# Optimization experiments

Measured on AMD Instinct MI355X. Metric: run time of the kernel, lower is better.

The kernel has to match this reference:

```python
import jax, jax.numpy as jnp
import numpy as np

H = 2048      # hidden_size
C = 256       # controller_hidden
B = 8192      # batch (tokens)
DT = 0.1


def setup_inputs() -> dict:
    key = jax.random.key(0)
    ks = jax.random.split(key, 8)
    h = jax.random.normal(ks[0], (B, H), dtype=jnp.float32)
    v = jax.random.normal(ks[1], (B, H), dtype=jnp.float32)
    # controller_in: Linear(2H -> C)
    W_in = jax.random.normal(ks[2], (C, 2 * H), dtype=jnp.float32) / np.sqrt(2 * H)
    b_in = jax.random.normal(ks[3], (C,), dtype=jnp.float32) * 0.01
    # controller_out: Linear(C -> 3H), weight ~ N(0, 0.01); bias init [2.2, -2.2, 0.0] per split
    W_out = jax.random.normal(ks[4], (3 * H, C), dtype=jnp.float32) * 0.01
    b_out = jnp.concatenate([
        jnp.full((H,), 2.2, dtype=jnp.float32),
        jnp.full((H,), -2.2, dtype=jnp.float32),
        jnp.zeros((H,), dtype=jnp.float32),
    ])
    # mu_proj: Linear(H -> H, bias=False); init zeros in module, use small random for a non-trivial baseline
    W_mu = jax.random.normal(ks[5], (H, H), dtype=jnp.float32) * 0.01
    mu = jnp.zeros((H,), dtype=jnp.float32)
    return {"h": h, "v": v, "W_in": W_in, "b_in": b_in, "W_out": W_out,
            "b_out": b_out, "W_mu": W_mu, "mu": mu}


def reference(h, v, W_in, b_in, W_out, b_out, W_mu, mu):
    hv = jnp.concatenate([h, v], axis=-1)                    # [B, 2H]
    ctrl = jax.nn.silu(hv @ W_in.T + b_in)                   # [B, C]
    ctrl_out = ctrl @ W_out.T + b_out                        # [B, 3H]
    alpha_raw, beta_raw, gate_raw = jnp.split(ctrl_out, 3, axis=-1)
    alpha = jax.nn.sigmoid(alpha_raw)
    beta = jnp.minimum(jax.nn.softplus(beta_raw), 2.0)
    gate = jax.nn.sigmoid(gate_raw)
    mu_contextual = mu + h @ W_mu.T                          # [B, H]
    error = h - mu_contextual
    v_next = jnp.clip(alpha * v - beta * error, -10.0, 10.0)
    h_next = h + DT * gate * v_next
    return h_next, v_next, mu_contextual
```

## Files before the change

### kernel.cpp

```cpp
#include <hip/hip_runtime.h>
#include <cstdint>
#include <cstddef>

#define B_TOK 8192
#define HDIM  2048
#define CDIM  256
#define KHV   4096
#define N3H   6144
#define DT_C  0.1f

typedef __bf16 bf16x8 __attribute__((ext_vector_type(8)));
typedef float  f32x4  __attribute__((ext_vector_type(4)));

typedef __attribute__((address_space(1))) void as1_void;
typedef __attribute__((address_space(3))) void as3_void;

__device__ __forceinline__ void g2l16(const void* g, void* l) {
    __builtin_amdgcn_global_load_lds((as1_void*)(void*)(uintptr_t)(g),
                                     (as3_void*)l, 16, 0, 0);
}

__device__ __forceinline__ unsigned short f2bf(float f) {
    unsigned int u = __float_as_uint(f);
    u += 0x7fffu + ((u >> 16) & 1u);
    return (unsigned short)(u >> 16);
}

__device__ __forceinline__ float bf2f(unsigned short s) {
    return __uint_as_float((unsigned int)s << 16);
}

__device__ __forceinline__ float fsigmoid(float x) {
    return __builtin_amdgcn_rcpf(1.f + __expf(-x));
}
__device__ __forceinline__ float fsoftplus(float x) {
    float t = __expf(-fabsf(x));
    return fmaxf(x, 0.f) + 0.69314718056f * __log2f(1.f + t);
}

__global__ void k_convert(const float* __restrict__ hp, const float* __restrict__ vp,
                          const float* __restrict__ Win, const float* __restrict__ Wout,
                          const float* __restrict__ Wmu,
                          ushort4* __restrict__ hv_b, ushort4* __restrict__ Wmu_b,
                          ushort4* __restrict__ Wout_b, ushort4* __restrict__ Win_b)
{
    const int HV_V   = B_TOK * KHV / 4;
    const int WMU_V  = HDIM * HDIM / 4;
    const int WOUT_V = N3H * CDIM / 4;
    const int WIN_V  = CDIM * KHV / 4;
    const int TOT    = HV_V + WMU_V + WOUT_V + WIN_V;
    for (int i = blockIdx.x * blockDim.x + threadIdx.x; i < TOT;
         i += gridDim.x * blockDim.x) {
        float4 x;
        ushort4* dst;
        if (i < HV_V) {
            int b  = i >> 10;
            int c4 = i & 1023;
            x = (c4 < 512) ? ((const float4*)hp)[b * 512 + c4]
                           : ((const float4*)vp)[b * 512 + (c4 - 512)];
            dst = hv_b + i;
        } else if (i < HV_V + WMU_V) {
            int j = i - HV_V;
            x = ((const float4*)Wmu)[j];
            dst = Wmu_b + j;
        } else if (i < HV_V + WMU_V + WOUT_V) {
            int j = i - (HV_V + WMU_V);
            x = ((const float4*)Wout)[j];
            dst = Wout_b + j;
        } else {
            int j = i - (HV_V + WMU_V + WOUT_V);
            x = ((const float4*)Win)[j];
            dst = Win_b + j;
        }
        ushort4 o;
        o.x = f2bf(x.x); o.y = f2bf(x.y); o.z = f2bf(x.z); o.w = f2bf(x.w);
        *dst = o;
    }
}

__global__ __launch_bounds__(256, 2)
void k_mid(const unsigned short* __restrict__ hvb,
           const unsigned short* __restrict__ Winb,
           const unsigned short* __restrict__ Wmub,
           const float* __restrict__ b_in,
           const float* __restrict__ mu,
           unsigned short* __restrict__ ctrl,
           float* __restrict__ outmu)
{
    __shared__ unsigned short sA[128 * 32];
    __shared__ unsigned short sB[128 * 32];
    const int tid  = threadIdx.x;
    const int wid  = tid >> 6;
    const int lane = tid & 63;
    const int quad = lane >> 4;
    const int l15  = lane & 15;
    const int wm   = wid >> 1, wn = wid & 1;
    const int srow = lane >> 2;
    const int sk   = (lane & 3) * 8;

    if (blockIdx.x < 512) {
        const int s  = (blockIdx.x & 7) * 64 + (blockIdx.x >> 3);
        const int bm = (s >> 2) * 64;
        const int bn = (s & 3) * 64;

        f32x4 acc[2][2];
#pragma unroll
        for (int a = 0; a < 2; ++a)
#pragma unroll
            for (int b = 0; b < 2; ++b) acc[a][b] = (f32x4){0.f, 0.f, 0.f, 0.f};

        const unsigned short* Ag = hvb  + (size_t)(bm + wid * 16 + srow) * KHV + sk;
        const unsigned short* Bg = Winb + (size_t)(bn + wid * 16 + srow) * KHV + sk;
        unsigned short* lA = &sA[(wid * 16) * 32];
        unsigned short* lB = &sB[(wid * 16) * 32];

        for (int kt = 0; kt < KHV; kt += 32) {
            g2l16(Ag + kt, lA);
            g2l16(Bg + kt, lB);
            __syncthreads();
            bf16x8 aF[2], bF[2];
#pragma unroll
            for (int t = 0; t < 2; ++t)
                aF[t] = *(const bf16x8*)&sA[(wm * 32 + t * 16 + l15) * 32 + quad * 8];
#pragma unroll
            for (int t = 0; t < 2; ++t)
                bF[t] = *(const bf16x8*)&sB[(wn * 32 + t * 16 + l15) * 32 + quad * 8];
#pragma unroll
            for (int tm = 0; tm < 2; ++tm)
#pragma unroll
                for (int tn = 0; tn < 2; ++tn)
                    acc[tm][tn] = __builtin_amdgcn_mfma_f32_16x16x32_bf16(
                        aF[tm], bF[tn], acc[tm][tn], 0, 0, 0);
            __syncthreads();
        }

#pragma unroll
        for (int tm = 0; tm < 2; ++tm)
#pragma unroll
            for (int tn = 0; tn < 2; ++tn) {
                const int n = bn + wn * 32 + tn * 16 + l15;
                const float bias = b_in[n];
#pragma unroll
                for (int r = 0; r < 4; ++r) {
                    const int m = bm + wm * 32 + tm * 16 + quad * 4 + r;
                    float x = acc[tm][tn][r] + bias;
                    float s2 = x * fsigmoid(x);
                    ctrl[(size_t)m * CDIM + n] = f2bf(s2);
                }
            }
    } else {
        const int t3  = blockIdx.x - 512;
        const int t3s = (t3 & 7) * 128 + (t3 >> 3);
        const int bm  = (t3s & 63) * 128;
        const int bn  = (t3s >> 6) * 128;

        f32x4 acc[4][4];
#pragma unroll
        for (int a = 0; a < 4; ++a)
#pragma unroll
            for (int b = 0; b < 4; ++b) acc[a][b] = (f32x4){0.f, 0.f, 0.f, 0.f};

        const unsigned short* Ag0 = hvb  + (size_t)(bm + wid * 16 + srow) * KHV + sk;
        const unsigned short* Ag1 = hvb  + (size_t)(bm + (wid + 4) * 16 + srow) * KHV + sk;
        const unsigned short* Bg0 = Wmub + (size_t)(bn + wid * 16 + srow) * HDIM + sk;
        const unsigned short* Bg1 = Wmub + (size_t)(bn + (wid + 4) * 16 + srow) * HDIM + sk;
        unsigned short* lA0 = &sA[(wid * 16) * 32];
        unsigned short* lA1 = &sA[((wid + 4) * 16) * 32];
        unsigned short* lB0 = &sB[(wid * 16) * 32];
        unsigned short* lB1 = &sB[((wid + 4) * 16) * 32];

        for (int kt = 0; kt < HDIM; kt += 32) {
            g2l16(Ag0 + kt, lA0);
            g2l16(Ag1 + kt, lA1);
            g2l16(Bg0 + kt, lB0);
            g2l16(Bg1 + kt, lB1);
            __syncthreads();
            bf16x8 aF[4], bF[4];
#pragma unroll
            for (int t = 0; t < 4; ++t)
                aF[t] = *(const bf16x8*)&sA[(wm * 64 + t * 16 + l15) * 32 + quad * 8];
#pragma unroll
            for (int t = 0; t < 4; ++t)
                bF[t] = *(const bf16x8*)&sB[(wn * 64 + t * 16 + l15) * 32 + quad * 8];
#pragma unroll
            for (int tm = 0; tm < 4; ++tm)
#pragma unroll
                for (int tn = 0; tn < 4; ++tn)
                    acc[tm][tn] = __builtin_amdgcn_mfma_f32_16x16x32_bf16(
                        aF[tm], bF[tn], acc[tm][tn], 0, 0, 0);
            __syncthreads();
        }

#pragma unroll
        for (int tm = 0; tm < 4; ++tm)
#pragma unroll
            for (int tn = 0; tn < 4; ++tn) {
                const int n = bn + wn * 64 + tn * 16 + l15;
                const float mub = mu[n];
#pragma unroll
                for (int r = 0; r < 4; ++r) {
                    const int m = bm + wm * 64 + tm * 16 + quad * 4 + r;
                    outmu[(size_t)m * HDIM + n] = acc[tm][tn][r] + mub;
                }
            }
    }
}

__global__ __launch_bounds__(256, 4)
void k_gemm2(const unsigned short* __restrict__ A,
             const unsigned short* __restrict__ Bw,
             const float* __restrict__ b_out,
             const unsigned short* __restrict__ hv,
             const float* __restrict__ mu_ctx,
             float* __restrict__ outp)
{
    __shared__ unsigned short sA[64 * 32];
    __shared__ unsigned short sB[3][64 * 32];
    const int tid  = threadIdx.x;
    const int wid  = tid >> 6;
    const int lane = tid & 63;
    const int quad = lane >> 4;
    const int l15  = lane & 15;
    const int wm   = wid >> 1, wn = wid & 1;
    const int bm   = blockIdx.x * 64;
    const int bn   = blockIdx.y * 64;
    const int srow = lane >> 2;
    const int sk   = (lane & 3) * 8;

    f32x4 acc[3][2][2];
#pragma unroll
    for (int p = 0; p < 3; ++p)
#pragma unroll
        for (int a = 0; a < 2; ++a)
#pragma unroll
            for (int b = 0; b < 2; ++b) acc[p][a][b] = (f32x4){0.f, 0.f, 0.f, 0.f};

    const unsigned short* Ag  = A + (size_t)(bm + wid * 16 + srow) * CDIM + sk;
    const unsigned short* Bg0 = Bw + (size_t)(0 * HDIM + bn + wid * 16 + srow) * CDIM + sk;
    const unsigned short* Bg1 = Bw + (size_t)(1 * HDIM + bn + wid * 16 + srow) * CDIM + sk;
    const unsigned short* Bg2 = Bw + (size_t)(2 * HDIM + bn + wid * 16 + srow) * CDIM + sk;
    unsigned short* lA  = &sA[(wid * 16) * 32];
    unsigned short* lB0 = &sB[0][(wid * 16) * 32];
    unsigned short* lB1 = &sB[1][(wid * 16) * 32];
    unsigned short* lB2 = &sB[2][(wid * 16) * 32];

    for (int kt = 0; kt < CDIM; kt += 32) {
        g2l16(Ag  + kt, lA);
        g2l16(Bg0 + kt, lB0);
        g2l16(Bg1 + kt, lB1);
        g2l16(Bg2 + kt, lB2);
        __syncthreads();
        bf16x8 aF[2], bF[3][2];
#pragma unroll
        for (int t = 0; t < 2; ++t)
            aF[t] = *(const bf16x8*)&sA[(wm * 32 + t * 16 + l15) * 32 + quad * 8];
#pragma unroll
        for (int p = 0; p < 3; ++p)
#pragma unroll
            for (int t = 0; t < 2; ++t)
                bF[p][t] = *(const bf16x8*)&sB[p][(wn * 32 + t * 16 + l15) * 32 + quad * 8];
#pragma unroll
        for (int p = 0; p < 3; ++p)
#pragma unroll
            for (int tm = 0; tm < 2; ++tm)
#pragma unroll
                for (int tn = 0; tn < 2; ++tn)
                    acc[p][tm][tn] = __builtin_amdgcn_mfma_f32_16x16x32_bf16(
                        aF[tm], bF[p][tn], acc[p][tm][tn], 0, 0, 0);
        __syncthreads();
    }

#pragma unroll
    for (int tm = 0; tm < 2; ++tm)
#pragma unroll
        for (int tn = 0; tn < 2; ++tn) {
            const int i  = bn + wn * 32 + tn * 16 + l15;
            const float ba = b_out[i];
            const float bb = b_out[HDIM + i];
            const float bg = b_out[2 * HDIM + i];
#pragma unroll
            for (int r = 0; r < 4; ++r) {
                const int m = bm + wm * 32 + tm * 16 + quad * 4 + r;
                const size_t off = (size_t)m * HDIM + i;
                const float araw = acc[0][tm][tn][r] + ba;
                const float braw = acc[1][tm][tn][r] + bb;
                const float graw = acc[2][tm][tn][r] + bg;
                const float alpha = fsigmoid(araw);
                const float beta  = fminf(fsoftplus(braw), 2.f);
                const float gate  = fsigmoid(graw);
                const float hh = bf2f(hv[(size_t)m * KHV + i]);
                const float vv = bf2f(hv[(size_t)m * KHV + HDIM + i]);
                const float mm = mu_ctx[off];
                const float err = hh - mm;
                float vn = alpha * vv - beta * err;
                vn = fminf(fmaxf(vn, -10.f), 10.f);
                const float hn = hh + DT_C * gate * vn;
                outp[off] = hn;
                outp[(size_t)B_TOK * HDIM + off] = vn;
            }
        }
}

extern "C" void kernel_launch(void* const* d_in, const int* in_sizes, int n_in,
                              void* d_out, int out_size, void* d_ws, size_t ws_size,
                              hipStream_t stream)
{
    const float* hp    = (const float*)d_in[0];
    const float* vp    = (const float*)d_in[1];
    const float* Win   = (const float*)d_in[2];
    const float* b_in  = (const float*)d_in[3];
    const float* Wout  = (const float*)d_in[4];
    const float* b_out = (const float*)d_in[5];
    const float* Wmu   = (const float*)d_in[6];
    const float* mu    = (const float*)d_in[7];
    float* outp = (float*)d_out;

    char* ws = (char*)d_ws;
    size_t off = 0;
    unsigned short* hv_b   = (unsigned short*)(ws + off); off += (size_t)B_TOK * KHV * 2;
    unsigned short* Wmu_b  = (unsigned short*)(ws + off); off += (size_t)HDIM * HDIM * 2;
    unsigned short* Wout_b = (unsigned short*)(ws + off); off += (size_t)N3H * CDIM * 2;
    unsigned short* Win_b  = (unsigned short*)(ws + off); off += (size_t)CDIM * KHV * 2;
    unsigned short* ctrl   = (unsigned short*)(ws + off); off += (size_t)B_TOK * CDIM * 2;

    k_convert<<<dim3(4096), dim3(256), 0, stream>>>(
        hp, vp, Win, Wout, Wmu,
        (ushort4*)hv_b, (ushort4*)Wmu_b, (ushort4*)Wout_b, (ushort4*)Win_b);

    k_mid<<<dim3(1536), dim3(256), 0, stream>>>(
        hv_b, Win_b, Wmu_b, b_in, mu, ctrl, outp + (size_t)2 * B_TOK * HDIM);

    k_gemm2<<<dim3(128, 32), dim3(256), 0, stream>>>(
        ctrl, Wout_b, b_out, hv_b,
        outp + (size_t)2 * B_TOK * HDIM, outp);
}
```

Baseline: 507.2 us.

## Double-buffer LDS tiles in all GEMMs, swizzle ctrl GEMM, interleave block types

```diff
diff --git a/kernel.cpp b/kernel.cpp
--- a/kernel.cpp
+++ b/kernel.cpp
@@ -73,7 +73,10 @@
             dst = Win_b + j;
         }
         ushort4 o;
-        o.x = f2bf(x.x); o.y = f2bf(x.y); o.z = f2bf(x.z); o.w = f2bf(x.w);
+        o.x = __builtin_bit_cast(unsigned short, (__bf16)x.x);
+        o.y = __builtin_bit_cast(unsigned short, (__bf16)x.y);
+        o.z = __builtin_bit_cast(unsigned short, (__bf16)x.z);
+        o.w = __builtin_bit_cast(unsigned short, (__bf16)x.w);
         *dst = o;
     }
 }
@@ -87,19 +90,21 @@
            unsigned short* __restrict__ ctrl,
            float* __restrict__ outmu)
 {
-    __shared__ unsigned short sA[128 * 32];
-    __shared__ unsigned short sB[128 * 32];
+    __shared__ unsigned short sA[2][4096];
+    __shared__ unsigned short sB[2][4096];
     const int tid  = threadIdx.x;
     const int wid  = tid >> 6;
     const int lane = tid & 63;
     const int quad = lane >> 4;
     const int l15  = lane & 15;
     const int wm   = wid >> 1, wn = wid & 1;
-    const int srow = lane >> 2;
-    const int sk   = (lane & 3) * 8;
-
-    if (blockIdx.x < 512) {
-        const int s  = (blockIdx.x & 7) * 64 + (blockIdx.x >> 3);
+
+    const unsigned int bidx = blockIdx.x;
+    const unsigned int r3   = bidx % 3u;
+
+    if (r3 == 0u) {
+        const int g1 = (int)(bidx / 3u);
+        const int s  = (g1 & 7) * 64 + (g1 >> 3);
         const int bm = (s >> 2) * 64;
         const int bn = (s & 3) * 64;
 
@@ -109,30 +114,50 @@
 #pragma unroll
             for (int b = 0; b < 2; ++b) acc[a][b] = (f32x4){0.f, 0.f, 0.f, 0.f};
 
-        const unsigned short* Ag = hvb  + (size_t)(bm + wid * 16 + srow) * KHV + sk;
-        const unsigned short* Bg = Winb + (size_t)(bn + wid * 16 + srow) * KHV + sk;
-        unsigned short* lA = &sA[(wid * 16) * 32];
-        unsigned short* lB = &sB[(wid * 16) * 32];
-
-        for (int kt = 0; kt < KHV; kt += 32) {
-            g2l16(Ag + kt, lA);
-            g2l16(Bg + kt, lB);
+        const int r8  = lane >> 3;
+        const int swz = ((lane & 7) ^ r8) * 8;
+        const unsigned short* Ag0 = hvb  + (size_t)(bm + (wid * 2    ) * 8 + r8) * KHV + swz;
+        const unsigned short* Ag1 = hvb  + (size_t)(bm + (wid * 2 + 1) * 8 + r8) * KHV + swz;
+        const unsigned short* Bg0 = Winb + (size_t)(bn + (wid * 2    ) * 8 + r8) * KHV + swz;
+        const unsigned short* Bg1 = Winb + (size_t)(bn + (wid * 2 + 1) * 8 + r8) * KHV + swz;
+
+        auto stage = [&](int cb, int kt) {
+            g2l16(Ag0 + kt, &sA[cb][(wid * 2    ) * 512]);
+            g2l16(Ag1 + kt, &sA[cb][(wid * 2 + 1) * 512]);
+            g2l16(Bg0 + kt, &sB[cb][(wid * 2    ) * 512]);
+            g2l16(Bg1 + kt, &sB[cb][(wid * 2 + 1) * 512]);
+        };
+        auto compute = [&](int cb) {
+            bf16x8 aF[2][2], bF[2][2];
+#pragma unroll
+            for (int kk = 0; kk < 2; ++kk) {
+                const int ca = (((kk * 4 + quad) ^ (l15 & 7)) * 8);
+#pragma unroll
+                for (int t = 0; t < 2; ++t) {
+                    aF[kk][t] = *(const bf16x8*)&sA[cb][(wm * 32 + t * 16 + l15) * 64 + ca];
+                    bF[kk][t] = *(const bf16x8*)&sB[cb][(wn * 32 + t * 16 + l15) * 64 + ca];
+                }
+            }
+#pragma unroll
+            for (int kk = 0; kk < 2; ++kk)
+#pragma unroll
+                for (int tm = 0; tm < 2; ++tm)
+#pragma unroll
+                    for (int tn = 0; tn < 2; ++tn)
+                        acc[tm][tn] = __builtin_amdgcn_mfma_f32_16x16x32_bf16(
+                            aF[kk][tm], bF[kk][tn], acc[tm][tn], 0, 0, 0);
+        };
+
+        stage(0, 0);
+        __syncthreads();
+        int cur = 0;
+        for (int kt = 64; kt < KHV; kt += 64) {
+            stage(cur ^ 1, kt);
+            compute(cur);
             __syncthreads();
-            bf16x8 aF[2], bF[2];
-#pragma unroll
-            for (int t = 0; t < 2; ++t)
-                aF[t] = *(const bf16x8*)&sA[(wm * 32 + t * 16 + l15) * 32 + quad * 8];
-#pragma unroll
-            for (int t = 0; t < 2; ++t)
-                bF[t] = *(const bf16x8*)&sB[(wn * 32 + t * 16 + l15) * 32 + quad * 8];
-#pragma unroll
-            for (int tm = 0; tm < 2; ++tm)
-#pragma unroll
-                for (int tn = 0; tn < 2; ++tn)
-                    acc[tm][tn] = __builtin_amdgcn_mfma_f32_16x16x32_bf16(
-                        aF[tm], bF[tn], acc[tm][tn], 0, 0, 0);
-            __syncthreads();
+            cur ^= 1;
         }
+        compute(cur);
 
 #pragma unroll
         for (int tm = 0; tm < 2; ++tm)
@@ -149,8 +174,8 @@
                 }
             }
     } else {
-        const int t3  = blockIdx.x - 512;
-        const int t3s = (t3 & 7) * 128 + (t3 >> 3);
+        const int g3  = (int)(bidx / 3u) * 2 + (int)r3 - 1;
+        const int t3s = (g3 & 7) * 128 + (g3 >> 3);
         const int bm  = (t3s & 63) * 128;
         const int bn  = (t3s >> 6) * 128;
 
@@ -160,36 +185,45 @@
 #pragma unroll
             for (int b = 0; b < 4; ++b) acc[a][b] = (f32x4){0.f, 0.f, 0.f, 0.f};
 
+        const int srow = lane >> 2;
+        const int sk   = (lane & 3) * 8;
         const unsigned short* Ag0 = hvb  + (size_t)(bm + wid * 16 + srow) * KHV + sk;
         const unsigned short* Ag1 = hvb  + (size_t)(bm + (wid + 4) * 16 + srow) * KHV + sk;
         const unsigned short* Bg0 = Wmub + (size_t)(bn + wid * 16 + srow) * HDIM + sk;
         const unsigned short* Bg1 = Wmub + (size_t)(bn + (wid + 4) * 16 + srow) * HDIM + sk;
-        unsigned short* lA0 = &sA[(wid * 16) * 32];
-        unsigned short* lA1 = &sA[((wid + 4) * 16) * 32];
-        unsigned short* lB0 = &sB[(wid * 16) * 32];
-        unsigned short* lB1 = &sB[((wid + 4) * 16) * 32];
-
-        for (int kt = 0; kt < HDIM; kt += 32) {
-            g2l16(Ag0 + kt, lA0);
-            g2l16(Ag1 + kt, lA1);
-            g2l16(Bg0 + kt, lB0);
-            g2l16(Bg1 + kt, lB1);
-            __syncthreads();
+
+        auto stage = [&](int cb, int kt) {
+            g2l16(Ag0 + kt, &sA[cb][(wid * 16) * 32]);
+            g2l16(Ag1 + kt, &sA[cb][((wid + 4) * 16) * 32]);
+            g2l16(Bg0 + kt, &sB[cb][(wid * 16) * 32]);
+            g2l16(Bg1 + kt, &sB[cb][((wid + 4) * 16) * 32]);
+        };
+        auto compute = [&](int cb) {
             bf16x8 aF[4], bF[4];
 #pragma unroll
             for (int t = 0; t < 4; ++t)
-                aF[t] = *(const bf16x8*)&sA[(wm * 64 + t * 16 + l15) * 32 + quad * 8];
+                aF[t] = *(const bf16x8*)&sA[cb][(wm * 64 + t * 16 + l15) * 32 + quad * 8];
 #pragma unroll
             for (int t = 0; t < 4; ++t)
-                bF[t] = *(const bf16x8*)&sB[(wn * 64 + t * 16 + l15) * 32 + quad * 8];
+                bF[t] = *(const bf16x8*)&sB[cb][(wn * 64 + t * 16 + l15) * 32 + quad * 8];
 #pragma unroll
             for (int tm = 0; tm < 4; ++tm)
 #pragma unroll
                 for (int tn = 0; tn < 4; ++tn)
                     acc[tm][tn] = __builtin_amdgcn_mfma_f32_16x16x32_bf16(
                         aF[tm], bF[tn], acc[tm][tn], 0, 0, 0);
+        };
+
+        stage(0, 0);
+        __syncthreads();
+        int cur = 0;
+        for (int kt = 32; kt < HDIM; kt += 32) {
+            stage(cur ^ 1, kt);
+            compute(cur);
             __syncthreads();
+            cur ^= 1;
         }
+        compute(cur);
 
 #pragma unroll
         for (int tm = 0; tm < 4; ++tm)
@@ -214,8 +248,8 @@
              const float* __restrict__ mu_ctx,
              float* __restrict__ outp)
 {
-    __shared__ unsigned short sA[64 * 32];
-    __shared__ unsigned short sB[3][64 * 32];
+    __shared__ unsigned short sA[2][2048];
+    __shared__ unsigned short sB[2][3][2048];
     const int tid  = threadIdx.x;
     const int wid  = tid >> 6;
     const int lane = tid & 63;
@@ -239,26 +273,23 @@
     const unsigned short* Bg0 = Bw + (size_t)(0 * HDIM + bn + wid * 16 + srow) * CDIM + sk;
     const unsigned short* Bg1 = Bw + (size_t)(1 * HDIM + bn + wid * 16 + srow) * CDIM + sk;
     const unsigned short* Bg2 = Bw + (size_t)(2 * HDIM + bn + wid * 16 + srow) * CDIM + sk;
-    unsigned short* lA  = &sA[(wid * 16) * 32];
-    unsigned short* lB0 = &sB[0][(wid * 16) * 32];
-    unsigned short* lB1 = &sB[1][(wid * 16) * 32];
-    unsigned short* lB2 = &sB[2][(wid * 16) * 32];
-
-    for (int kt = 0; kt < CDIM; kt += 32) {
-        g2l16(Ag  + kt, lA);
-        g2l16(Bg0 + kt, lB0);
-        g2l16(Bg1 + kt, lB1);
-        g2l16(Bg2 + kt, lB2);
-        __syncthreads();
+
+    auto stage = [&](int cb, int kt) {
+        g2l16(Ag  + kt, &sA[cb][(wid * 16) * 32]);
+        g2l16(Bg0 + kt, &sB[cb][0][(wid * 16) * 32]);
+        g2l16(Bg1 + kt, &sB[cb][1][(wid * 16) * 32]);
+        g2l16(Bg2 + kt, &sB[cb][2][(wid * 16) * 32]);
+    };
+    auto compute = [&](int cb) {
         bf16x8 aF[2], bF[3][2];
 #pragma unroll
         for (int t = 0; t < 2; ++t)
-            aF[t] = *(const bf16x8*)&sA[(wm * 32 + t * 16 + l15) * 32 + quad * 8];
+            aF[t] = *(const bf16x8*)&sA[cb][(wm * 32 + t * 16 + l15) * 32 + quad * 8];
 #pragma unroll
         for (int p = 0; p < 3; ++p)
 #pragma unroll
             for (int t = 0; t < 2; ++t)
-                bF[p][t] = *(const bf16x8*)&sB[p][(wn * 32 + t * 16 + l15) * 32 + quad * 8];
+                bF[p][t] = *(const bf16x8*)&sB[cb][p][(wn * 32 + t * 16 + l15) * 32 + quad * 8];
 #pragma unroll
         for (int p = 0; p < 3; ++p)
 #pragma unroll
@@ -267,8 +298,18 @@
                 for (int tn = 0; tn < 2; ++tn)
                     acc[p][tm][tn] = __builtin_amdgcn_mfma_f32_16x16x32_bf16(
                         aF[tm], bF[p][tn], acc[p][tm][tn], 0, 0, 0);
+    };
+
+    stage(0, 0);
+    __syncthreads();
+    int cur = 0;
+    for (int kt = 32; kt < CDIM; kt += 32) {
+        stage(cur ^ 1, kt);
+        compute(cur);
         __syncthreads();
+        cur ^= 1;
     }
+    compute(cur);
 
 #pragma unroll
     for (int tm = 0; tm < 2; ++tm)
```

After: 539.9 us. 6.4% more time.

## Double-buffer LDS staging in k_mid GEMMs with vmcnt-based pipelining

Applied to the files above, without the earlier changes.

```diff
diff --git a/kernel.cpp b/kernel.cpp
--- a/kernel.cpp
+++ b/kernel.cpp
@@ -14,6 +14,9 @@
 
 typedef __attribute__((address_space(1))) void as1_void;
 typedef __attribute__((address_space(3))) void as3_void;
+
+#define VM_WAIT(N) asm volatile("s_waitcnt vmcnt(" #N ")" ::: "memory")
+#define SCHED_FENCE() __builtin_amdgcn_sched_barrier(0)
 
 __device__ __forceinline__ void g2l16(const void* g, void* l) {
     __builtin_amdgcn_global_load_lds((as1_void*)(void*)(uintptr_t)(g),
@@ -73,7 +76,10 @@
             dst = Win_b + j;
         }
         ushort4 o;
-        o.x = f2bf(x.x); o.y = f2bf(x.y); o.z = f2bf(x.z); o.w = f2bf(x.w);
+        o.x = __builtin_bit_cast(unsigned short, (__bf16)x.x);
+        o.y = __builtin_bit_cast(unsigned short, (__bf16)x.y);
+        o.z = __builtin_bit_cast(unsigned short, (__bf16)x.z);
+        o.w = __builtin_bit_cast(unsigned short, (__bf16)x.w);
         *dst = o;
     }
 }
@@ -87,8 +93,8 @@
            unsigned short* __restrict__ ctrl,
            float* __restrict__ outmu)
 {
-    __shared__ unsigned short sA[128 * 32];
-    __shared__ unsigned short sB[128 * 32];
+    __shared__ unsigned short sA[2][4096];
+    __shared__ unsigned short sB[2][4096];
     const int tid  = threadIdx.x;
     const int wid  = tid >> 6;
     const int lane = tid & 63;
@@ -99,7 +105,7 @@
     const int sk   = (lane & 3) * 8;
 
     if (blockIdx.x < 512) {
-        const int s  = (blockIdx.x & 7) * 64 + (blockIdx.x >> 3);
+        const int s  = ((int)blockIdx.x & 7) * 64 + ((int)blockIdx.x >> 3);
         const int bm = (s >> 2) * 64;
         const int bn = (s & 3) * 64;
 
@@ -111,28 +117,44 @@
 
         const unsigned short* Ag = hvb  + (size_t)(bm + wid * 16 + srow) * KHV + sk;
         const unsigned short* Bg = Winb + (size_t)(bn + wid * 16 + srow) * KHV + sk;
-        unsigned short* lA = &sA[(wid * 16) * 32];
-        unsigned short* lB = &sB[(wid * 16) * 32];
-
-        for (int kt = 0; kt < KHV; kt += 32) {
-            g2l16(Ag + kt, lA);
-            g2l16(Bg + kt, lB);
-            __syncthreads();
+
+        auto stage = [&](int cb, int t) {
+            g2l16(Ag + t * 32, &sA[cb][(wid * 16) * 32]);
+            g2l16(Bg + t * 32, &sB[cb][(wid * 16) * 32]);
+        };
+        auto compute = [&](int cb) {
             bf16x8 aF[2], bF[2];
 #pragma unroll
             for (int t = 0; t < 2; ++t)
-                aF[t] = *(const bf16x8*)&sA[(wm * 32 + t * 16 + l15) * 32 + quad * 8];
+                aF[t] = *(const bf16x8*)&sA[cb][(wm * 32 + t * 16 + l15) * 32 + quad * 8];
 #pragma unroll
             for (int t = 0; t < 2; ++t)
-                bF[t] = *(const bf16x8*)&sB[(wn * 32 + t * 16 + l15) * 32 + quad * 8];
+                bF[t] = *(const bf16x8*)&sB[cb][(wn * 32 + t * 16 + l15) * 32 + quad * 8];
 #pragma unroll
             for (int tm = 0; tm < 2; ++tm)
 #pragma unroll
                 for (int tn = 0; tn < 2; ++tn)
                     acc[tm][tn] = __builtin_amdgcn_mfma_f32_16x16x32_bf16(
                         aF[tm], bF[tn], acc[tm][tn], 0, 0, 0);
-            __syncthreads();
+        };
+
+        const int nt = KHV / 32;
+        stage(0, 0);
+        stage(1, 1);
+        for (int t = 0; t < nt - 1; ++t) {
+            VM_WAIT(2);
+            __builtin_amdgcn_s_barrier();
+            SCHED_FENCE();
+            compute(t & 1);
+            SCHED_FENCE();
+            __builtin_amdgcn_s_barrier();
+            SCHED_FENCE();
+            if (t + 2 < nt) stage(t & 1, t + 2);
         }
+        VM_WAIT(0);
+        __builtin_amdgcn_s_barrier();
+        SCHED_FENCE();
+        compute((nt - 1) & 1);
 
 #pragma unroll
         for (int tm = 0; tm < 2; ++tm)
@@ -149,7 +171,7 @@
                 }
             }
     } else {
-        const int t3  = blockIdx.x - 512;
+        const int t3  = (int)blockIdx.x - 512;
         const int t3s = (t3 & 7) * 128 + (t3 >> 3);
         const int bm  = (t3s & 63) * 128;
         const int bn  = (t3s >> 6) * 128;
@@ -164,32 +186,46 @@
         const unsigned short* Ag1 = hvb  + (size_t)(bm + (wid + 4) * 16 + srow) * KHV + sk;
         const unsigned short* Bg0 = Wmub + (size_t)(bn + wid * 16 + srow) * HDIM + sk;
         const unsigned short* Bg1 = Wmub + (size_t)(bn + (wid + 4) * 16 + srow) * HDIM + sk;
-        unsigned short* lA0 = &sA[(wid * 16) * 32];
-        unsigned short* lA1 = &sA[((wid + 4) * 16) * 32];
-        unsigned short* lB0 = &sB[(wid * 16) * 32];
-        unsigned short* lB1 = &sB[((wid + 4) * 16) * 32];
-
-        for (int kt = 0; kt < HDIM; kt += 32) {
-            g2l16(Ag0 + kt, lA0);
-            g2l16(Ag1 + kt, lA1);
-            g2l16(Bg0 + kt, lB0);
-            g2l16(Bg1 + kt, lB1);
-            __syncthreads();
+
+        auto stage = [&](int cb, int t) {
+            g2l16(Ag0 + t * 32, &sA[cb][(wid * 16) * 32]);
+            g2l16(Ag1 + t * 32, &sA[cb][((wid + 4) * 16) * 32]);
+            g2l16(Bg0 + t * 32, &sB[cb][(wid * 16) * 32]);
+            g2l16(Bg1 + t * 32, &sB[cb][((wid + 4) * 16) * 32]);
+        };
+        auto compute = [&](int cb) {
             bf16x8 aF[4], bF[4];
 #pragma unroll
             for (int t = 0; t < 4; ++t)
-                aF[t] = *(const bf16x8*)&sA[(wm * 64 + t * 16 + l15) * 32 + quad * 8];
+                aF[t] = *(const bf16x8*)&sA[cb][(wm * 64 + t * 16 + l15) * 32 + quad * 8];
 #pragma unroll
             for (int t = 0; t < 4; ++t)
-                bF[t] = *(const bf16x8*)&sB[(wn * 64 + t * 16 + l15) * 32 + quad * 8];
+                bF[t] = *(const bf16x8*)&sB[cb][(wn * 64 + t * 16 + l15) * 32 + quad * 8];
 #pragma unroll
             for (int tm = 0; tm < 4; ++tm)
 #pragma unroll
                 for (int tn = 0; tn < 4; ++tn)
                     acc[tm][tn] = __builtin_amdgcn_mfma_f32_16x16x32_bf16(
                         aF[tm], bF[tn], acc[tm][tn], 0, 0, 0);
-            __syncthreads();
+        };
+
+        const int nt = HDIM / 32;
+        stage(0, 0);
+        stage(1, 1);
+        for (int t = 0; t < nt - 1; ++t) {
+            VM_WAIT(4);
+            __builtin_amdgcn_s_barrier();
+            SCHED_FENCE();
+            compute(t & 1);
+            SCHED_FENCE();
+            __builtin_amdgcn_s_barrier();
+            SCHED_FENCE();
+            if (t + 2 < nt) stage(t & 1, t + 2);
         }
+        VM_WAIT(0);
+        __builtin_amdgcn_s_barrier();
+        SCHED_FENCE();
+        compute((nt - 1) & 1);
 
 #pragma unroll
         for (int tm = 0; tm < 4; ++tm)
```

Result: no change. 516.5 us (+1.8%).
